# Kernel tuning notes

Measured on AMD Instinct MI355X. Metric: run time of the kernel, lower is better.

The kernel has to match this reference:

```python
import jax, jax.numpy as jnp
import numpy as np

B, S, D = 2, 2048, 1024
H = 16
DH = D // H


def setup_inputs() -> dict:
    key = jax.random.key(0)
    ks = jax.random.split(key, 6)
    scale = 1.0 / np.sqrt(D)
    x = jax.random.normal(ks[0], (B, S, D), dtype=jnp.float32)
    Wq = jax.random.normal(ks[1], (D, D), dtype=jnp.float32) * scale
    Wk = jax.random.normal(ks[2], (D, D), dtype=jnp.float32) * scale
    Wv = jax.random.normal(ks[3], (D, D), dtype=jnp.float32) * scale
    Wo = jax.random.normal(ks[4], (D, D), dtype=jnp.float32) * scale
    bo = jax.random.normal(ks[5], (D,), dtype=jnp.float32) * 0.01
    return {"x": x, "Wq": Wq, "Wk": Wk, "Wv": Wv, "Wo": Wo, "bo": bo}


def reference(x, Wq, Wk, Wv, Wo, bo):
    b, t, _ = x.shape
    # project and split heads: [b, h, t, dh]
    q = (x @ Wq).reshape(b, t, H, DH).transpose(0, 2, 1, 3)
    k = (x @ Wk).reshape(b, t, H, DH).transpose(0, 2, 1, 3)
    v = (x @ Wv).reshape(b, t, H, DH).transpose(0, 2, 1, 3)
    scores = jnp.einsum('bhqd,bhkd->bhqk', q, k)
    causal = jnp.triu(jnp.ones((t, t), dtype=bool), k=1)
    scores = jnp.where(causal, -jnp.inf, scores)
    attn = jax.nn.softmax(scores / np.sqrt(DH), axis=-1)
    ctx = jnp.einsum('bhqk,bhkd->bhqd', attn, v)
    ctx = ctx.transpose(0, 2, 1, 3).reshape(b, t, D)
    return ctx @ Wo + bo
```

## Files before the change

kernel.cpp:

```cpp
#include <hip/hip_runtime.h>
#include <hip/hip_bf16.h>

#define B 2
#define S 2048
#define D 1024
#define NH 16
#define DH 64
#define M (B*S)
#define BQ 64
#define BK 64
#define KSCALE 0.18033688011112042f

typedef __hip_bfloat16 bf16;
typedef __attribute__((ext_vector_type(8))) short frag_ab;
typedef __attribute__((ext_vector_type(4))) float frag_cd;
typedef unsigned long long ull;

__device__ __forceinline__ void gload_lds16(const bf16* g, bf16* l) {
    __builtin_amdgcn_global_load_lds((const __attribute__((address_space(1))) unsigned int*)g,
                                     (__attribute__((address_space(3))) unsigned int*)l,
                                     16, 0, 0);
}

__global__ __launch_bounds__(256) void prep(const float* __restrict__ x,  bf16* __restrict__ xb,
                                            const float* __restrict__ W0, const float* __restrict__ W1,
                                            const float* __restrict__ W2, const float* __restrict__ W3,
                                            bf16* __restrict__ T0, bf16* __restrict__ T1,
                                            bf16* __restrict__ T2, bf16* __restrict__ T3) {
    if (blockIdx.z == 4) {
        const int l = blockIdx.y * 32 + blockIdx.x;
        int i = (l * 256 + threadIdx.x) * 4;
#pragma unroll
        for (int rep = 0; rep < 4; rep++, i += 1024 * 256 * 4) {
            const float4 v = *(const float4*)(x + i);
            __align__(8) bf16 t4[4] = {__float2bfloat16(v.x), __float2bfloat16(v.y),
                                       __float2bfloat16(v.z), __float2bfloat16(v.w)};
            *(ull*)(xb + i) = *(const ull*)t4;
        }
        return;
    }
    const float* src; bf16* dst;
    switch (blockIdx.z) {
        case 0: src = W0; dst = T0; break;
        case 1: src = W1; dst = T1; break;
        case 2: src = W2; dst = T2; break;
        default: src = W3; dst = T3; break;
    }
    __shared__ float t[32][33];
    const int tx = threadIdx.x & 31, ty = threadIdx.x >> 5;
    const int c0 = blockIdx.x * 32, r0 = blockIdx.y * 32;
#pragma unroll
    for (int i = 0; i < 4; i++)
        t[ty + 8 * i][tx] = src[(size_t)(r0 + ty + 8 * i) * D + c0 + tx];
    __syncthreads();
#pragma unroll
    for (int i = 0; i < 4; i++)
        dst[(size_t)(c0 + ty + 8 * i) * D + r0 + tx] = __float2bfloat16(t[tx][ty + 8 * i]);
}

__global__ __launch_bounds__(256) void gemm_qkv_all(const bf16* __restrict__ A, const bf16* __restrict__ Bt,
                                                    bf16* __restrict__ Qb, bf16* __restrict__ Kb,
                                                    bf16* __restrict__ Vt_g) {
    __shared__ __align__(16) bf16 As[128 * BK];
    __shared__ __align__(16) bf16 Bs[128 * BK];
    const int tid = threadIdx.x, wave = tid >> 6, lane = tid & 63;
    const int r16 = lane & 15, quad = lane >> 4;
    const int row0 = blockIdx.y * 128;
    const int col0 = blockIdx.x * 128;
    const int wm = (wave & 1) * 64, wn = (wave >> 1) * 64;

    frag_cd acc[4][4];
#pragma unroll
    for (int mt = 0; mt < 4; mt++)
#pragma unroll
        for (int nt = 0; nt < 4; nt++) acc[mt][nt] = frag_cd{0.f, 0.f, 0.f, 0.f};

    for (int k0 = 0; k0 < D; k0 += BK) {
        __syncthreads();
#pragma unroll
        for (int j = 0; j < 4; j++) {
            const int s = wave * 256 + j * 64 + lane;
            const int r = s >> 3;
            const int c = (s ^ r) & 7;
            gload_lds16(A  + (size_t)(row0 + r) * D + k0 + c * 8, &As[(wave * 256 + j * 64) * 8]);
            gload_lds16(Bt + (size_t)(col0 + r) * D + k0 + c * 8, &Bs[(wave * 256 + j * 64) * 8]);
        }
        __syncthreads();

        frag_ab af[4][2], bf[4][2];
#pragma unroll
        for (int mt = 0; mt < 4; mt++) {
            const int row = wm + mt * 16 + r16;
#pragma unroll
            for (int ks = 0; ks < 2; ks++)
                af[mt][ks] = *(const frag_ab*)&As[row * 64 + (((ks * 4 + quad) ^ (row & 7)) * 8)];
        }
#pragma unroll
        for (int nt = 0; nt < 4; nt++) {
            const int row = wn + nt * 16 + r16;
#pragma unroll
            for (int ks = 0; ks < 2; ks++)
                bf[nt][ks] = *(const frag_ab*)&Bs[row * 64 + (((ks * 4 + quad) ^ (row & 7)) * 8)];
        }
#pragma unroll
        for (int mt = 0; mt < 4; mt++)
#pragma unroll
            for (int nt = 0; nt < 4; nt++)
#pragma unroll
                for (int ks = 0; ks < 2; ks++)
                    acc[mt][nt] = __builtin_amdgcn_mfma_f32_16x16x32_bf16(
                        af[mt][ks], bf[nt][ks], acc[mt][nt], 0, 0, 0);
    }

    const int third = col0 >> 10;
    if (third < 2) {
        bf16* Out = (third == 0) ? Qb : Kb;
        const float sc = (third == 0) ? KSCALE : 1.f;
#pragma unroll
        for (int mt = 0; mt < 4; mt++)
#pragma unroll
            for (int nt = 0; nt < 4; nt++) {
                const int cl = (col0 + wn + nt * 16 + r16) & 1023;
#pragma unroll
                for (int rg = 0; rg < 4; rg++) {
                    const int row = row0 + wm + mt * 16 + quad * 4 + rg;
                    Out[(size_t)row * D + cl] = __float2bfloat16(acc[mt][nt][rg] * sc);
                }
            }
    } else {
        const int bb = row0 >> 11;
        const int sb0 = (row0 & 2047) + wm;
#pragma unroll
        for (int mt = 0; mt < 4; mt++)
#pragma unroll
            for (int nt = 0; nt < 4; nt++) {
                const int c  = (col0 + wn + nt * 16 + r16) - 2048;
                const int hh = c >> 6, dl = c & 63;
                const int sb = sb0 + mt * 16 + quad * 4;
                __align__(8) bf16 t4[4];
#pragma unroll
                for (int rg = 0; rg < 4; rg++) t4[rg] = __float2bfloat16(acc[mt][nt][rg]);
                *(ull*)(Vt_g + (((size_t)bb * 16 + hh) * 64 + dl) * S + sb) = *(const ull*)t4;
            }
    }
}

__global__ __launch_bounds__(256) void attn_mfma(const bf16* __restrict__ Q,
                                                 const bf16* __restrict__ K,
                                                 const bf16* __restrict__ Vg,
                                                 bf16* __restrict__ Ctx) {
    __shared__ __align__(16) bf16 Ks[2][BK * DH];
    __shared__ __align__(16) bf16 Vt[2][BK * DH];
    __shared__ __align__(16) bf16 Qs[BQ * DH];
    bf16* Ps = Qs;

    const int tid = threadIdx.x, wave = tid >> 6, lane = tid & 63;
    const int r16 = lane & 15, quad = lane >> 4;
    const int bh = blockIdx.x, jy = blockIdx.y;
    const int qt = (jy < 16) ? jy : 47 - jy;
    const int b = bh >> 4, h = bh & 15;
    const size_t base  = (size_t)b * S * D + (size_t)h * DH;
    const size_t vbase = (size_t)bh * DH * S;
    const int q0 = qt * BQ;
    const int qwave = q0 + wave * 16;
    const int nkt = qt + 1;

#pragma unroll
    for (int j = 0; j < 2; j++) {
        const int s = wave * 128 + j * 64 + lane;
        const int r = s >> 3, c = (s ^ r) & 7;
        gload_lds16(Q + base + (size_t)(q0 + r) * D + c * 8, &Qs[(wave * 128 + j * 64) * 8]);
    }
#pragma unroll
    for (int j = 0; j < 2; j++) {
        const int s = wave * 128 + j * 64 + lane;
        const int r = s >> 3, c = (s ^ r) & 7;
        gload_lds16(K  + base  + (size_t)r * D + c * 8, &Ks[0][(wave * 128 + j * 64) * 8]);
        gload_lds16(Vg + vbase + (size_t)r * S + c * 8, &Vt[0][(wave * 128 + j * 64) * 8]);
    }
    __syncthreads();

    frag_ab qf[2];
    {
        const int row = wave * 16 + r16;
#pragma unroll
        for (int ks = 0; ks < 2; ks++)
            qf[ks] = *(const frag_ab*)&Qs[row * 64 + (((ks * 4 + quad) ^ (row & 7)) * 8)];
    }

    float mrun = -1e30f, lrun = 0.f;
    frag_cd Oacc[4];
#pragma unroll
    for (int nd = 0; nd < 4; nd++) Oacc[nd] = frag_cd{0.f, 0.f, 0.f, 0.f};

    for (int kt = 0; kt < nkt; kt++) {
        const int k0  = kt * BK;
        const int cur = kt & 1;

        if (kt + 1 < nkt) {
            const int kn = k0 + BK;
#pragma unroll
            for (int j = 0; j < 2; j++) {
                const int s = wave * 128 + j * 64 + lane;
                const int r = s >> 3, c = (s ^ r) & 7;
                gload_lds16(K  + base  + (size_t)(kn + r) * D + c * 8,
                            &Ks[cur ^ 1][(wave * 128 + j * 64) * 8]);
                gload_lds16(Vg + vbase + (size_t)r * S + kn + c * 8,
                            &Vt[cur ^ 1][(wave * 128 + j * 64) * 8]);
            }
        }

        {
            frag_ab ka[4][2];
#pragma unroll
            for (int mk = 0; mk < 4; mk++) {
                const int row = mk * 16 + r16;
#pragma unroll
                for (int ks = 0; ks < 2; ks++)
                    ka[mk][ks] = *(const frag_ab*)&Ks[cur][row * 64 + (((ks * 4 + quad) ^ (row & 7)) * 8)];
            }
            const bool domask = (k0 + BK - 1 > qwave);

            frag_cd Sc[4];
#pragma unroll
            for (int mk = 0; mk < 4; mk++) {
                Sc[mk] = frag_cd{0.f, 0.f, 0.f, 0.f};
#pragma unroll
                for (int ks = 0; ks < 2; ks++)
                    Sc[mk] = __builtin_amdgcn_mfma_f32_16x16x32_bf16(
                        ka[mk][ks], qf[ks], Sc[mk], 0, 0, 0);
            }
            const int qg = qwave + r16;
            float mx = -1e30f;
#pragma unroll
            for (int mk = 0; mk < 4; mk++)
#pragma unroll
                for (int rg = 0; rg < 4; rg++) {
                    float sv = Sc[mk][rg];
                    if (domask) {
                        const int keyg = k0 + mk * 16 + quad * 4 + rg;
                        sv = (keyg <= qg) ? sv : -1e30f;
                    }
                    Sc[mk][rg] = sv;
                    mx = fmaxf(mx, sv);
                }
            mx = fmaxf(mx, __shfl_xor(mx, 16, 64));
            mx = fmaxf(mx, __shfl_xor(mx, 32, 64));
            const float mnew  = fmaxf(mrun, mx);
            const float alpha = __builtin_amdgcn_exp2f(mrun - mnew);
            mrun = mnew;
            float rs = 0.f;
#pragma unroll
            for (int mk = 0; mk < 4; mk++)
#pragma unroll
                for (int rg = 0; rg < 4; rg++) {
                    const float pv = __builtin_amdgcn_exp2f(Sc[mk][rg] - mnew);
                    Sc[mk][rg] = pv;
                    rs += pv;
                }
            rs += __shfl_xor(rs, 16, 64);
            rs += __shfl_xor(rs, 32, 64);
            lrun = lrun * alpha + rs;

            const int qrow = wave * 16 + r16;
#pragma unroll
            for (int mk = 0; mk < 4; mk++) {
                __align__(8) bf16 t4[4];
#pragma unroll
                for (int rg = 0; rg < 4; rg++) t4[rg] = __float2bfloat16(Sc[mk][rg]);
                const int g = (mk * 4 + quad) ^ r16;
                *(ull*)&Ps[qrow * 64 + g * 4] = *(const ull*)t4;
            }
#pragma unroll
            for (int nd = 0; nd < 4; nd++)
#pragma unroll
                for (int rg = 0; rg < 4; rg++) Oacc[nd][rg] *= alpha;


            frag_ab pa[2], vb[4][2];
#pragma unroll
            for (int ks = 0; ks < 2; ks++) {
                const int gb = ks * 8 + quad * 2;
                union { ull u[2]; frag_ab f; } t;
                t.u[0] = *(const ull*)&Ps[qrow * 64 + ((gb    ) ^ r16) * 4];
                t.u[1] = *(const ull*)&Ps[qrow * 64 + ((gb + 1) ^ r16) * 4];
                pa[ks] = t.f;
            }
#pragma unroll
            for (int nd = 0; nd < 4; nd++) {
                const int row = nd * 16 + r16;
#pragma unroll
                for (int ks = 0; ks < 2; ks++)
                    vb[nd][ks] = *(const frag_ab*)&Vt[cur][row * 64 + (((ks * 4 + quad) ^ (row & 7)) * 8)];
            }
#pragma unroll
            for (int nd = 0; nd < 4; nd++)
#pragma unroll
                for (int ks = 0; ks < 2; ks++)
                    Oacc[nd] = __builtin_amdgcn_mfma_f32_16x16x32_bf16(
                        vb[nd][ks], pa[ks], Oacc[nd], 0, 0, 0);
        }

        __syncthreads();
    }

    {
        const float invl = 1.f / lrun;
        const int qg = qwave + r16;
#pragma unroll
        for (int nd = 0; nd < 4; nd++) {
            __align__(8) bf16 t4[4];
#pragma unroll
            for (int rg = 0; rg < 4; rg++)
                t4[rg] = __float2bfloat16(Oacc[nd][rg] * invl);
            *(ull*)(Ctx + base + (size_t)qg * D + nd * 16 + quad * 4) = *(const ull*)t4;
        }
    }
}

__global__ __launch_bounds__(256) void gemm_out64(const bf16* __restrict__ A, const bf16* __restrict__ Bt,
                                                  const float* __restrict__ bias, float* __restrict__ Out) {
    __shared__ __align__(16) bf16 As[2][64 * BK];
    __shared__ __align__(16) bf16 Bs[2][128 * BK];
    const int tid = threadIdx.x, wave = tid >> 6, lane = tid & 63;
    const int r16 = lane & 15, quad = lane >> 4;
    const int row0 = blockIdx.y * 64;
    const int col0 = blockIdx.x * 128;
    const int wm = (wave & 1) * 32, wn = (wave >> 1) * 64;

    frag_cd acc[2][4];
#pragma unroll
    for (int mt = 0; mt < 2; mt++)
#pragma unroll
        for (int nt = 0; nt < 4; nt++) acc[mt][nt] = frag_cd{0.f, 0.f, 0.f, 0.f};

#pragma unroll
    for (int j = 0; j < 2; j++) {
        const int s = wave * 128 + j * 64 + lane;
        const int r = s >> 3, c = (s ^ r) & 7;
        gload_lds16(A + (size_t)(row0 + r) * D + c * 8, &As[0][(wave * 128 + j * 64) * 8]);
    }
#pragma unroll
    for (int j = 0; j < 4; j++) {
        const int s = wave * 256 + j * 64 + lane;
        const int r = s >> 3, c = (s ^ r) & 7;
        gload_lds16(Bt + (size_t)(col0 + r) * D + c * 8, &Bs[0][(wave * 256 + j * 64) * 8]);
    }
    __syncthreads();

    for (int kt = 0; kt < D / BK; kt++) {
        const int cur = kt & 1;
        if (kt + 1 < D / BK) {
            const int kn = (kt + 1) * BK;
#pragma unroll
            for (int j = 0; j < 2; j++) {
                const int s = wave * 128 + j * 64 + lane;
                const int r = s >> 3, c = (s ^ r) & 7;
                gload_lds16(A + (size_t)(row0 + r) * D + kn + c * 8,
                            &As[cur ^ 1][(wave * 128 + j * 64) * 8]);
            }
#pragma unroll
            for (int j = 0; j < 4; j++) {
                const int s = wave * 256 + j * 64 + lane;
                const int r = s >> 3, c = (s ^ r) & 7;
                gload_lds16(Bt + (size_t)(col0 + r) * D + kn + c * 8,
                            &Bs[cur ^ 1][(wave * 256 + j * 64) * 8]);
            }
        }

        frag_ab af[2][2], bf[4][2];
#pragma unroll
        for (int mt = 0; mt < 2; mt++) {
            const int row = wm + mt * 16 + r16;
#pragma unroll
            for (int ks = 0; ks < 2; ks++)
                af[mt][ks] = *(const frag_ab*)&As[cur][row * 64 + (((ks * 4 + quad) ^ (row & 7)) * 8)];
        }
#pragma unroll
        for (int nt = 0; nt < 4; nt++) {
            const int row = wn + nt * 16 + r16;
#pragma unroll
            for (int ks = 0; ks < 2; ks++)
                bf[nt][ks] = *(const frag_ab*)&Bs[cur][row * 64 + (((ks * 4 + quad) ^ (row & 7)) * 8)];
        }
#pragma unroll
        for (int mt = 0; mt < 2; mt++)
#pragma unroll
            for (int nt = 0; nt < 4; nt++)
#pragma unroll
                for (int ks = 0; ks < 2; ks++)
                    acc[mt][nt] = __builtin_amdgcn_mfma_f32_16x16x32_bf16(
                        af[mt][ks], bf[nt][ks], acc[mt][nt], 0, 0, 0);

        __syncthreads();
    }

#pragma unroll
    for (int mt = 0; mt < 2; mt++)
#pragma unroll
        for (int nt = 0; nt < 4; nt++) {
            const int col = col0 + wn + nt * 16 + r16;
            const float bv = bias[col];
#pragma unroll
            for (int rg = 0; rg < 4; rg++) {
                const int row = row0 + wm + mt * 16 + quad * 4 + rg;
                Out[(size_t)row * D + col] = acc[mt][nt][rg] + bv;
            }
        }
}

extern "C" void kernel_launch(void* const* d_in, const int* in_sizes, int n_in,
                              void* d_out, int out_size, void* d_ws, size_t ws_size,
                              hipStream_t stream) {
    const float* x  = (const float*)d_in[0];
    const float* Wq = (const float*)d_in[1];
    const float* Wk = (const float*)d_in[2];
    const float* Wv = (const float*)d_in[3];
    const float* Wo = (const float*)d_in[4];
    const float* bo = (const float*)d_in[5];
    float* out = (float*)d_out;

    bf16* xb    = (bf16*)d_ws;
    bf16* WqkvT = xb    + (size_t)M * D;
    bf16* WoT   = WqkvT + (size_t)3 * D * D;
    bf16* Qb    = WoT   + (size_t)D * D;
    bf16* Kb    = Qb    + (size_t)M * D;
    bf16* Vt_g  = Kb    + (size_t)M * D;
    bf16* Ctxb  = Vt_g  + (size_t)M * D;

    prep<<<dim3(32, 32, 5), 256, 0, stream>>>(x, xb, Wq, Wk, Wv, Wo,
                                              WqkvT, WqkvT + (size_t)D * D,
                                              WqkvT + (size_t)2 * D * D, WoT);
    gemm_qkv_all<<<dim3(24, 32), 256, 0, stream>>>(xb, WqkvT, Qb, Kb, Vt_g);
    attn_mfma<<<dim3(B * NH, S / BQ), 256, 0, stream>>>(Qb, Kb, Vt_g, Ctxb);
    gemm_out64<<<dim3(8, 64), 256, 0, stream>>>(Ctxb, WoT, bo, out);
}
```

Measured before the change: 183.5 us.

## Split long causal query tiles across two blocks with in-kernel partial-softmax merge

Attention work is redistributed so each query tile in the upper half is processed by two blocks covering separate key ranges, giving 1536 blocks with more even per-block work than the previous 1024. The first block to finish writes its unnormalized output, running max and running sum to a workspace slot. The second block spins on a ready flag, then merges the two partial softmax states before writing the context. Counters and flags are zeroed in the prep kernel. The spin-wait relies on the partner block being scheduled, and it adds global traffic and atomics.

```diff
diff --git a/kernel.cpp b/kernel.cpp
--- a/kernel.cpp
+++ b/kernel.cpp
@@ -26,9 +26,13 @@
                                             const float* __restrict__ W0, const float* __restrict__ W1,
                                             const float* __restrict__ W2, const float* __restrict__ W3,
                                             bf16* __restrict__ T0, bf16* __restrict__ T1,
-                                            bf16* __restrict__ T2, bf16* __restrict__ T3) {
+                                            bf16* __restrict__ T2, bf16* __restrict__ T3,
+                                            int* __restrict__ flags) {
     if (blockIdx.z == 4) {
         const int l = blockIdx.y * 32 + blockIdx.x;
+        if (l == 0) {
+            ((int4*)flags)[threadIdx.x] = int4{0, 0, 0, 0};
+        }
         int i = (l * 256 + threadIdx.x) * 4;
 #pragma unroll
         for (int rep = 0; rep < 4; rep++, i += 1024 * 256 * 4) {
@@ -148,7 +152,10 @@
 __global__ __launch_bounds__(256) void attn_mfma(const bf16* __restrict__ Q,
                                                  const bf16* __restrict__ K,
                                                  const bf16* __restrict__ Vg,
-                                                 bf16* __restrict__ Ctx) {
+                                                 bf16* __restrict__ Ctx,
+                                                 float* __restrict__ Opart,
+                                                 int* __restrict__ cnt,
+                                                 int* __restrict__ ready) {
     __shared__ __align__(16) bf16 Ks[2][BK * DH];
     __shared__ __align__(16) bf16 Vt[2][BK * DH];
     __shared__ __align__(16) bf16 Qs[BQ * DH];
@@ -156,14 +163,23 @@
 
     const int tid = threadIdx.x, wave = tid >> 6, lane = tid & 63;
     const int r16 = lane & 15, quad = lane >> 4;
-    const int bh = blockIdx.x, jy = blockIdx.y;
-    const int qt = (jy < 16) ? jy : 47 - jy;
+
+    const int id = blockIdx.x;
+    const int bh = id & 31;
+    const int g  = id >> 5;
+    int qt, ktb, kte;
+    bool partial;
+    if (g < 16)      { qt = 16 + g;        ktb = 0;  kte = 15; partial = true;  }
+    else if (g < 24) { qt = 15 - (g - 16); ktb = 0;  kte = qt; partial = false; }
+    else if (g < 32) { qt = 31 - (g - 24); ktb = 16; kte = qt; partial = true;  }
+    else if (g < 40) { qt = 23 - (g - 32); ktb = 16; kte = qt; partial = true;  }
+    else             { qt = 7  - (g - 40); ktb = 0;  kte = qt; partial = false; }
+
     const int b = bh >> 4, h = bh & 15;
     const size_t base  = (size_t)b * S * D + (size_t)h * DH;
     const size_t vbase = (size_t)bh * DH * S;
     const int q0 = qt * BQ;
     const int qwave = q0 + wave * 16;
-    const int nkt = qt + 1;
 
 #pragma unroll
     for (int j = 0; j < 2; j++) {
@@ -175,8 +191,8 @@
     for (int j = 0; j < 2; j++) {
         const int s = wave * 128 + j * 64 + lane;
         const int r = s >> 3, c = (s ^ r) & 7;
-        gload_lds16(K  + base  + (size_t)r * D + c * 8, &Ks[0][(wave * 128 + j * 64) * 8]);
-        gload_lds16(Vg + vbase + (size_t)r * S + c * 8, &Vt[0][(wave * 128 + j * 64) * 8]);
+        gload_lds16(K  + base  + (size_t)(ktb * BK + r) * D + c * 8, &Ks[0][(wave * 128 + j * 64) * 8]);
+        gload_lds16(Vg + vbase + (size_t)r * S + ktb * BK + c * 8,   &Vt[0][(wave * 128 + j * 64) * 8]);
     }
     __syncthreads();
 
@@ -193,11 +209,11 @@
 #pragma unroll
     for (int nd = 0; nd < 4; nd++) Oacc[nd] = frag_cd{0.f, 0.f, 0.f, 0.f};
 
-    for (int kt = 0; kt < nkt; kt++) {
+    for (int kt = ktb; kt <= kte; kt++) {
         const int k0  = kt * BK;
         const int cur = kt & 1;
 
-        if (kt + 1 < nkt) {
+        if (kt < kte) {
             const int kn = k0 + BK;
 #pragma unroll
             for (int j = 0; j < 2; j++) {
@@ -268,8 +284,8 @@
                 __align__(8) bf16 t4[4];
 #pragma unroll
                 for (int rg = 0; rg < 4; rg++) t4[rg] = __float2bfloat16(Sc[mk][rg]);
-                const int g = (mk * 4 + quad) ^ r16;
-                *(ull*)&Ps[qrow * 64 + g * 4] = *(const ull*)t4;
+                const int g2 = (mk * 4 + quad) ^ r16;
+                *(ull*)&Ps[qrow * 64 + g2 * 4] = *(const ull*)t4;
             }
 #pragma unroll
             for (int nd = 0; nd < 4; nd++)
@@ -304,9 +320,11 @@
         __syncthreads();
     }
 
-    {
+    const int qlocal = wave * 16 + r16;
+
+    if (!partial) {
         const float invl = 1.f / lrun;
-        const int qg = qwave + r16;
+        const int qg = q0 + qlocal;
 #pragma unroll
         for (int nd = 0; nd < 4; nd++) {
             __align__(8) bf16 t4[4];
@@ -315,6 +333,53 @@
                 t4[rg] = __float2bfloat16(Oacc[nd][rg] * invl);
             *(ull*)(Ctx + base + (size_t)qg * D + nd * 16 + quad * 4) = *(const ull*)t4;
         }
+        return;
+    }
+
+    const int slot = bh * 16 + (qt - 16);
+    float* Op = Opart + (size_t)slot * 4224;
+    int* flag_sh = (int*)Qs;
+    if (tid == 0) flag_sh[0] = atomicAdd(&cnt[slot], 1);
+    __syncthreads();
+    const int oldv = flag_sh[0];
+
+    if (oldv == 0) {
+#pragma unroll
+        for (int nd = 0; nd < 4; nd++)
+            *(float4*)(Op + qlocal * 64 + nd * 16 + quad * 4) =
+                float4{Oacc[nd][0], Oacc[nd][1], Oacc[nd][2], Oacc[nd][3]};
+        if (quad == 0) {
+            Op[4096 + qlocal] = mrun;
+            Op[4160 + qlocal] = lrun;
+        }
+        __syncthreads();
+        if (tid == 0)
+            __hip_atomic_store(&ready[slot], 1, __ATOMIC_RELEASE, __HIP_MEMORY_SCOPE_AGENT);
+        return;
+    }
+
+    if (tid == 0) {
+        while (__hip_atomic_load(&ready[slot], __ATOMIC_ACQUIRE, __HIP_MEMORY_SCOPE_AGENT) == 0)
+            __builtin_amdgcn_s_sleep(2);
+    }
+    __syncthreads();
+
+    const float mo = Op[4096 + qlocal];
+    const float lo = Op[4160 + qlocal];
+    const float mstar = fmaxf(mrun, mo);
+    const float fa = __builtin_amdgcn_exp2f(mrun - mstar);
+    const float fb = __builtin_amdgcn_exp2f(mo - mstar);
+    const float linv = 1.f / (lrun * fa + lo * fb);
+    const int qg = q0 + qlocal;
+#pragma unroll
+    for (int nd = 0; nd < 4; nd++) {
+        const float4 ov = *(const float4*)(Op + qlocal * 64 + nd * 16 + quad * 4);
+        const float o4[4] = {ov.x, ov.y, ov.z, ov.w};
+        __align__(8) bf16 t4[4];
+#pragma unroll
+        for (int rg = 0; rg < 4; rg++)
+            t4[rg] = __float2bfloat16((Oacc[nd][rg] * fa + o4[rg] * fb) * linv);
+        *(ull*)(Ctx + base + (size_t)qg * D + nd * 16 + quad * 4) = *(const ull*)t4;
     }
 }
 
@@ -427,11 +492,14 @@
     bf16* Kb    = Qb    + (size_t)M * D;
     bf16* Vt_g  = Kb    + (size_t)M * D;
     bf16* Ctxb  = Vt_g  + (size_t)M * D;
+    float* Opart = (float*)(Ctxb + (size_t)M * D);
+    int*   cnt   = (int*)(Opart + (size_t)512 * 4224);
+    int*   ready = cnt + 512;
 
     prep<<<dim3(32, 32, 5), 256, 0, stream>>>(x, xb, Wq, Wk, Wv, Wo,
                                               WqkvT, WqkvT + (size_t)D * D,
-                                              WqkvT + (size_t)2 * D * D, WoT);
+                                              WqkvT + (size_t)2 * D * D, WoT, cnt);
     gemm_qkv_all<<<dim3(24, 32), 256, 0, stream>>>(xb, WqkvT, Qb, Kb, Vt_g);
-    attn_mfma<<<dim3(B * NH, S / BQ), 256, 0, stream>>>(Qb, Kb, Vt_g, Ctxb);
+    attn_mfma<<<dim3(1536), 256, 0, stream>>>(Qb, Kb, Vt_g, Ctxb, Opart, cnt, ready);
     gemm_out64<<<dim3(8, 64), 256, 0, stream>>>(Ctxb, WoT, bo, out);
 }
```

Result: slower. 194.8 us (+6.1%).
